# Kernel tuning notes

Measured on AMD Instinct MI355X. Metric: run time of the kernel, lower is better.

## Reference

```python
import jax, jax.numpy as jnp
import numpy as np
import math

B, S, D = 2, 1024, 1024
H, KVH = 16, 4
HD = D // H            # 64
WIN = 256              # sliding window size
E, TOPK = 8, 2
DFF = 4096
T = B * S
CAP = max(1, int(1.0 * T / E))   # capacity_factor=1.0 -> 256
EPS = 1e-6
NEG_INF = float('-inf')


def setup_inputs() -> dict:
    key = jax.random.key(0)
    ks = jax.random.split(key, 10)
    x = jax.random.normal(ks[0], (B, S, D), dtype=jnp.float32)
    # causal additive mask (B,1,S,S)
    i = jnp.arange(S)[:, None]
    j = jnp.arange(S)[None, :]
    causal = jnp.where(j <= i, 0.0, NEG_INF).astype(jnp.float32)
    mask = jnp.broadcast_to(causal[None, None], (B, 1, S, S))
    global_token_mask = jax.random.uniform(ks[1], (B, S)) < 0.05
    sd = 1.0 / math.sqrt(D)
    Wq = jax.random.normal(ks[2], (D, D), jnp.float32) * sd
    Wk = jax.random.normal(ks[3], (D, D), jnp.float32) * sd
    Wv = jax.random.normal(ks[4], (D, D), jnp.float32) * sd
    Wo = jax.random.normal(ks[5], (D, D), jnp.float32) * sd
    g1 = jnp.ones((D,), jnp.float32)
    g2 = jnp.ones((D,), jnp.float32)
    Wgate = jax.random.normal(ks[6], (D, E), jnp.float32) * 0.02
    W1 = jax.random.normal(ks[7], (E, D, 2 * DFF), jnp.float32) * sd
    W2 = jax.random.normal(ks[8], (E, DFF, D), jnp.float32) * (1.0 / math.sqrt(DFF))
    return {"x": x, "mask": mask, "global_token_mask": global_token_mask,
            "Wq": Wq, "Wk": Wk, "Wv": Wv, "Wo": Wo,
            "g1": g1, "g2": g2, "Wgate": Wgate, "W1": W1, "W2": W2}


def _rope_tables():
    inv_freq = 1.0 / (10000.0 ** (jnp.arange(0, HD, 2, dtype=jnp.float32) / HD))
    t = jnp.arange(S, dtype=jnp.float32)
    freqs = t[:, None] * inv_freq[None, :]          # (S, HD/2)
    emb = jnp.concatenate([freqs, freqs], axis=-1)  # (S, HD)
    return emb[None, None].astype(jnp.float32), None  # placeholder


def _rotate_half(x):
    x1, x2 = jnp.split(x, 2, axis=-1)
    return jnp.concatenate([-x2, x1], axis=-1)


def _rmsnorm(x, g):
    return g * x * jax.lax.rsqrt(jnp.mean(x * x, axis=-1, keepdims=True) + EPS)


def _attention(x, mask, gtm, Wq, Wk, Wv, Wo):
    # The torch GQA view/permute chain reduces exactly to a plain head split.
    q = (x @ Wq).reshape(B, S, H, HD).transpose(0, 2, 1, 3)  # (B,H,S,HD)
    k = (x @ Wk).reshape(B, S, H, HD).transpose(0, 2, 1, 3)
    v = (x @ Wv).reshape(B, S, H, HD).transpose(0, 2, 1, 3)
    # inline RoPE
    inv_freq = 1.0 / (10000.0 ** (jnp.arange(0, HD, 2, dtype=jnp.float32) / HD))
    t = jnp.arange(S, dtype=jnp.float32)
    freqs = t[:, None] * inv_freq[None, :]
    emb = jnp.concatenate([freqs, freqs], axis=-1)  # (S,HD)
    cos = jnp.cos(emb)[None, None]
    sin = jnp.sin(emb)[None, None]
    q = q * cos + _rotate_half(q) * sin
    k = k * cos + _rotate_half(k) * sin
    scores = jnp.einsum('bhqd,bhkd->bhqk', q, k) / math.sqrt(HD)
    # sliding-window mask
    i = jnp.arange(S)[:, None]
    j = jnp.arange(S)[None, :]
    diff = i - j
    swa = jnp.where((diff < 0) | (diff >= WIN), NEG_INF, 0.0).astype(scores.dtype)
    combined = mask + swa[None, None]               # (B,1,S,S)
    gt = gtm[:, None, :, None]                      # query is global
    gs = gtm[:, None, None, :]                      # key is global
    combined = jnp.where(gt | gs, 0.0, combined)
    attn = jax.nn.softmax(scores + combined, axis=-1)
    out = jnp.einsum('bhqk,bhkd->bhqd', attn, v)
    out = out.transpose(0, 2, 1, 3).reshape(B, S, D)
    return out @ Wo


def _moe(x, Wgate, W1, W2):
    flat_x = x.reshape(T, D)
    gate_scores = jax.nn.softmax(flat_x @ Wgate, axis=-1)          # (T,E)
    topk_vals, topk_idx = jax.lax.top_k(gate_scores, TOPK)          # (T,k)
    phi_mean = jnp.mean(gate_scores, axis=0)
    aux_loss = E * jnp.sum(phi_mean * phi_mean)
    # per-token weight for each expert (0 if not routed)
    w = jnp.zeros((T, E), flat_x.dtype).at[jnp.arange(T)[:, None], topk_idx].add(topk_vals)
    # capacity: pick top-CAP tokens by weight per expert. Unrouted tokens have
    # weight 0 so any that slip in contribute exactly 0 (matches torch semantics).
    sel_w, sel_idx = jax.lax.top_k(w.T, CAP)                        # (E,CAP)
    tok = flat_x[sel_idx]                                           # (E,CAP,D)
    h = jnp.einsum('ecd,edf->ecf', tok, W1)                         # (E,CAP,2*DFF)
    h1, h2 = jnp.split(h, 2, axis=-1)
    act = h1 * jax.nn.silu(h2)                                      # SwiGLU
    out_e = jnp.einsum('ecf,efd->ecd', act, W2) * sel_w[..., None]
    combined = jnp.zeros((T, D), flat_x.dtype).at[sel_idx.reshape(-1)].add(out_e.reshape(-1, D))
    return combined.reshape(B, S, D), aux_loss


def reference(x, mask, global_token_mask, Wq, Wk, Wv, Wo, g1, g2, Wgate, W1, W2):
    # pre-norm residual block (SublayerConnection with RMSNorm, dropout=identity in eval)
    h = x + _attention(_rmsnorm(x, g1), mask, global_token_mask, Wq, Wk, Wv, Wo)
    moe_out, aux_loss = _moe(_rmsnorm(h, g2), Wgate, W1, W2)
    out = h + moe_out
    return out, aux_loss
```

## Files before the change

### kernel.cpp

```cpp
#include <hip/hip_runtime.h>
#include <hip/hip_bf16.h>
#include <math.h>

#define T_TOK 2048
#define DMODEL 1024
#define NH 16
#define HD 64
#define S_LEN 1024
#define NE 8
#define CAP 256
#define DFF 4096

typedef __attribute__((ext_vector_type(8))) short bf16x8;
typedef __attribute__((ext_vector_type(4))) float f32x4;

__device__ inline unsigned short f2bf(float f) {
    union { float f; unsigned int u; } x; x.f = f;
    unsigned int u = x.u;
    unsigned int r = (u + 0x7FFFu + ((u >> 16) & 1u)) >> 16;
    return (unsigned short)r;
}

__device__ inline float bf2f(unsigned short h) {
    union { unsigned int u; float f; } x; x.u = (unsigned int)h << 16; return x.f;
}

__device__ inline unsigned int pkbf(float lo, float hi) {
    __hip_bfloat162 h2 = __float22bfloat162_rn(make_float2(lo, hi));
    unsigned int r;
    __builtin_memcpy(&r, &h2, 4);
    return r;
}

__device__ inline void gload16(const void* g, void* l) {
    __builtin_amdgcn_global_load_lds(
        (const __attribute__((address_space(1))) unsigned int*)g,
        (__attribute__((address_space(3))) unsigned int*)l, 16, 0, 0);
}

__global__ void rope_table_kernel(float* __restrict__ rc, float* __restrict__ rs,
                                  float* __restrict__ gsum) {
    int s = blockIdx.x;
    int i = threadIdx.x;
    float invf = powf(10000.0f, -(float)(2 * i) / 64.0f);
    float ang = (float)s * invf;
    rc[s * 32 + i] = cosf(ang);
    rs[s * 32 + i] = sinf(ang);
    if (blockIdx.x == 0 && threadIdx.x < 8) gsum[threadIdx.x] = 0.f;
}

template <int OUTBF>
__global__ __launch_bounds__(256) void rmsnorm_kernel(const float* __restrict__ x,
                                                      const float* __restrict__ g,
                                                      void* __restrict__ yv) {
    __shared__ float red[256];
    int t = blockIdx.x;
    int tid = threadIdx.x;
    const float* xr = x + (size_t)t * DMODEL;
    float ss = 0.f;
    for (int d = tid; d < DMODEL; d += 256) { float v = xr[d]; ss += v * v; }
    red[tid] = ss; __syncthreads();
    for (int o = 128; o > 0; o >>= 1) { if (tid < o) red[tid] += red[tid + o]; __syncthreads(); }
    float scale = 1.0f / sqrtf(red[0] / (float)DMODEL + 1e-6f);
    if (OUTBF) {
        unsigned short* yr = (unsigned short*)yv + (size_t)t * DMODEL;
        for (int d = tid; d < DMODEL; d += 256) yr[d] = f2bf(g[d] * xr[d] * scale);
    } else {
        float* yr = (float*)yv + (size_t)t * DMODEL;
        for (int d = tid; d < DMODEL; d += 256) yr[d] = g[d] * xr[d] * scale;
    }
}

__global__ __launch_bounds__(256) void gemm_qkv_rope(const unsigned short* __restrict__ xn,
                                                     const float* __restrict__ Wq,
                                                     const float* __restrict__ Wk,
                                                     const float* __restrict__ Wv,
                                                     const float* __restrict__ rc,
                                                     const float* __restrict__ rs,
                                                     unsigned short* __restrict__ Qh,
                                                     unsigned short* __restrict__ Ql,
                                                     unsigned short* __restrict__ Kh,
                                                     unsigned short* __restrict__ Kl,
                                                     unsigned short* __restrict__ Vtb) {
    __shared__ unsigned short As[128 * 64];
    __shared__ unsigned int Bp[64 * 32];
    const int mat = blockIdx.x >> 4;
    const int h = blockIdx.x & 15;
    const float* B = ((mat == 0) ? Wq : (mat == 1) ? Wk : Wv) + h * 64;
    const int by = blockIdx.y * 128;
    const int tid = threadIdx.x, l = tid & 63, wid = tid >> 6;
    const int g = l >> 4;
    const int kp = tid >> 3;
    const int nc = tid & 7;
    const int chunk = kp >> 2, within = kp & 3;

    f32x4 acc[2][4] = {};

    const float* Brow = B + (size_t)(2 * kp) * 1024 + nc * 8;
    float4 a0 = *(const float4*)(Brow);
    float4 a1 = *(const float4*)(Brow + 4);
    float4 b0 = *(const float4*)(Brow + 1024);
    float4 b1 = *(const float4*)(Brow + 1028);

    for (int k0 = 0; k0 < 1024; k0 += 64) {
        #pragma unroll
        for (int i = 0; i < 4; i++) {
            int c = i * 256 + tid;
            int row = c >> 3, sl = c & 7, gs = sl ^ (row & 7);
            gload16(xn + (size_t)(by + row) * 1024 + k0 + gs * 8, &As[c * 8]);
        }
        unsigned int p[8];
        p[0] = pkbf(a0.x, b0.x); p[1] = pkbf(a0.y, b0.y);
        p[2] = pkbf(a0.z, b0.z); p[3] = pkbf(a0.w, b0.w);
        p[4] = pkbf(a1.x, b1.x); p[5] = pkbf(a1.y, b1.y);
        p[6] = pkbf(a1.z, b1.z); p[7] = pkbf(a1.w, b1.w);
        #pragma unroll
        for (int i = 0; i < 8; i++) {
            int n_loc = nc * 8 + i;
            int idx = n_loc * 32 + ((chunk ^ (n_loc & 7)) << 2) + within;
            Bp[idx] = p[i];
        }
        __syncthreads();
        if (k0 + 64 < 1024) {
            const float* Bn = B + (size_t)(k0 + 64 + 2 * kp) * 1024 + nc * 8;
            a0 = *(const float4*)(Bn);
            a1 = *(const float4*)(Bn + 4);
            b0 = *(const float4*)(Bn + 1024);
            b1 = *(const float4*)(Bn + 1028);
        }
        #pragma unroll
        for (int ks = 0; ks < 2; ks++) {
            bf16x8 af[2];
            #pragma unroll
            for (int m = 0; m < 2; m++) {
                int row = wid * 32 + m * 16 + (l & 15);
                int sl = (ks * 4 + g) ^ (row & 7);
                af[m] = *(const bf16x8*)&As[row * 64 + sl * 8];
            }
            #pragma unroll
            for (int nf = 0; nf < 4; nf++) {
                int n_loc = nf * 16 + (l & 15);
                int base = n_loc * 32 + (((ks * 4 + g) ^ (n_loc & 7)) << 2);
                bf16x8 bfr = *(const bf16x8*)&Bp[base];
                #pragma unroll
                for (int m = 0; m < 2; m++)
                    acc[m][nf] = __builtin_amdgcn_mfma_f32_16x16x32_bf16(af[m], bfr, acc[m][nf], 0, 0, 0);
            }
        }
        __syncthreads();
    }

    if (mat < 2) {
        unsigned short* Dh = (mat == 0) ? Qh : Kh;
        unsigned short* Dl = (mat == 0) ? Ql : Kl;
        float scale = (mat == 0) ? 0.125f : 1.0f;
        #pragma unroll
        for (int m = 0; m < 2; m++)
            #pragma unroll
            for (int r = 0; r < 4; r++) {
                int t = by + wid * 32 + m * 16 + g * 4 + r;
                int b = t >> 10, s = t & 1023;
                size_t ob = ((size_t)(b * 16 + h) * 1024 + s) * 64;
                #pragma unroll
                for (int pr = 0; pr < 2; pr++) {
                    int i = pr * 16 + (l & 15);
                    float c = rc[s * 32 + i], sn = rs[s * 32 + i];
                    float a = acc[m][pr][r], bb = acc[m][pr + 2][r];
                    float v0 = (a * c - bb * sn) * scale;
                    float v1 = (bb * c + a * sn) * scale;
                    unsigned short h0 = f2bf(v0), h1 = f2bf(v1);
                    Dh[ob + i] = h0;      Dl[ob + i] = f2bf(v0 - bf2f(h0));
                    Dh[ob + i + 32] = h1; Dl[ob + i + 32] = f2bf(v1 - bf2f(h1));
                }
            }
    } else {
        #pragma unroll
        for (int m = 0; m < 2; m++) {
            int t0 = by + wid * 32 + m * 16 + g * 4;
            int b = t0 >> 10, s0 = t0 & 1023;
            #pragma unroll
            for (int nf = 0; nf < 4; nf++) {
                int d = nf * 16 + (l & 15);
                unsigned short tmp[4];
                #pragma unroll
                for (int r = 0; r < 4; r++) tmp[r] = f2bf(acc[m][nf][r]);
                *(uint2*)&Vtb[((size_t)(b * 16 + h) * 64 + d) * 1024 + s0] = *(uint2*)tmp;
            }
        }
    }
}

template <int RES>
__global__ __launch_bounds__(256) void gemm_bf32(const unsigned short* __restrict__ A,
                                                 const float* __restrict__ B,
                                                 const float* __restrict__ Rr,
                                                 float* __restrict__ C,
                                                 int K, int lda,
                                                 long long sA, long long sB, long long sC) {
    __shared__ unsigned short As[128 * 64];
    __shared__ unsigned int Bp[32 * 32];
    A += (long long)blockIdx.z * sA + (long long)blockIdx.y * 128 * lda;
    B += (long long)blockIdx.z * sB;
    C += (long long)blockIdx.z * sC + (long long)blockIdx.y * 128 * 1024;
    const float* Rp = RES ? (Rr + (long long)blockIdx.y * 128 * 1024) : nullptr;
    const int bx = blockIdx.x * 32;
    const int tid = threadIdx.x, l = tid & 63, wid = tid >> 6;
    const int g = l >> 4;
    const int kp = tid >> 3;
    const int nc = tid & 7;
    const int chunk = kp >> 2, within = kp & 3;

    f32x4 acc[2][2] = {};

    const float* Brow = B + (size_t)(2 * kp) * 1024 + bx + nc * 4;
    float4 a0 = *(const float4*)(Brow);
    float4 a1 = *(const float4*)(Brow + 1024);

    for (int k0 = 0; k0 < K; k0 += 64) {
        #pragma unroll
        for (int i = 0; i < 4; i++) {
            int c = i * 256 + tid;
            int row = c >> 3, sl = c & 7, gs = sl ^ (row & 7);
            gload16(A + (size_t)row * lda + k0 + gs * 8, &As[c * 8]);
        }
        unsigned int p1[4];
        p1[0] = pkbf(a0.x, a1.x); p1[1] = pkbf(a0.y, a1.y);
        p1[2] = pkbf(a0.z, a1.z); p1[3] = pkbf(a0.w, a1.w);
        #pragma unroll
        for (int i = 0; i < 4; i++) {
            int n_loc = nc * 4 + i;
            int idx = n_loc * 32 + ((chunk ^ (n_loc & 7)) << 2) + within;
            Bp[idx] = p1[i];
        }
        __syncthreads();
        if (k0 + 64 < K) {
            const float* Bn = B + (size_t)(k0 + 64 + 2 * kp) * 1024 + bx + nc * 4;
            a0 = *(const float4*)(Bn);
            a1 = *(const float4*)(Bn + 1024);
        }
        #pragma unroll
        for (int ks = 0; ks < 2; ks++) {
            bf16x8 af[2];
            #pragma unroll
            for (int m = 0; m < 2; m++) {
                int row = wid * 32 + m * 16 + (l & 15);
                int sl = (ks * 4 + g) ^ (row & 7);
                af[m] = *(const bf16x8*)&As[row * 64 + sl * 8];
            }
            #pragma unroll
            for (int nf = 0; nf < 2; nf++) {
                int n_loc = nf * 16 + (l & 15);
                int base = n_loc * 32 + (((ks * 4 + g) ^ (n_loc & 7)) << 2);
                bf16x8 bfr = *(const bf16x8*)&Bp[base];
                #pragma unroll
                for (int m = 0; m < 2; m++)
                    acc[m][nf] = __builtin_amdgcn_mfma_f32_16x16x32_bf16(af[m], bfr, acc[m][nf], 0, 0, 0);
            }
        }
        __syncthreads();
    }
    #pragma unroll
    for (int m = 0; m < 2; m++) {
        int row0 = wid * 32 + m * 16 + g * 4;
        #pragma unroll
        for (int nf = 0; nf < 2; nf++) {
            int col = bx + nf * 16 + (l & 15);
            #pragma unroll
            for (int r = 0; r < 4; r++) {
                size_t idx = (size_t)(row0 + r) * 1024 + col;
                float v = acc[m][nf][r];
                if (RES) v += Rp[idx];
                C[idx] = v;
            }
        }
    }
}

__global__ __launch_bounds__(256) void gemm_w1_fused(const unsigned short* __restrict__ tok,
                                                     const float* __restrict__ W1,
                                                     unsigned short* __restrict__ act) {
    __shared__ unsigned short As[256 * 64];
    __shared__ unsigned int B1p[32 * 32];
    __shared__ unsigned int B2p[32 * 32];
    const int e = blockIdx.y;
    const int bx = blockIdx.x * 32;
    const unsigned short* A = tok + (size_t)e * CAP * DMODEL;
    const float* B = W1 + (size_t)e * DMODEL * (2 * DFF);
    unsigned short* C = act + (size_t)e * CAP * DFF;
    const int tid = threadIdx.x, l = tid & 63, wid = tid >> 6;
    const int g = l >> 4;
    const int kp = tid >> 3;
    const int nc = tid & 7;
    const int chunk = kp >> 2, within = kp & 3;

    f32x4 acc1[4][2] = {};
    f32x4 acc2[4][2] = {};

    const float* Brow = B + (size_t)(2 * kp) * 8192 + bx + nc * 4;
    float4 a0 = *(const float4*)(Brow);
    float4 a1 = *(const float4*)(Brow + 8192);
    float4 c0 = *(const float4*)(Brow + 4096);
    float4 c1 = *(const float4*)(Brow + 4096 + 8192);

    for (int k0 = 0; k0 < DMODEL; k0 += 64) {
        #pragma unroll
        for (int i = 0; i < 8; i++) {
            int c = i * 256 + tid;
            int row = c >> 3, sl = c & 7, gs = sl ^ (row & 7);
            gload16(A + (size_t)row * DMODEL + k0 + gs * 8, &As[c * 8]);
        }
        unsigned int p1[4], p2[4];
        p1[0] = pkbf(a0.x, a1.x); p1[1] = pkbf(a0.y, a1.y);
        p1[2] = pkbf(a0.z, a1.z); p1[3] = pkbf(a0.w, a1.w);
        p2[0] = pkbf(c0.x, c1.x); p2[1] = pkbf(c0.y, c1.y);
        p2[2] = pkbf(c0.z, c1.z); p2[3] = pkbf(c0.w, c1.w);
        #pragma unroll
        for (int i = 0; i < 4; i++) {
            int n_loc = nc * 4 + i;
            int idx = n_loc * 32 + ((chunk ^ (n_loc & 7)) << 2) + within;
            B1p[idx] = p1[i];
            B2p[idx] = p2[i];
        }
        __syncthreads();
        if (k0 + 64 < DMODEL) {
            const float* Bn = B + (size_t)(k0 + 64 + 2 * kp) * 8192 + bx + nc * 4;
            a0 = *(const float4*)(Bn);
            a1 = *(const float4*)(Bn + 8192);
            c0 = *(const float4*)(Bn + 4096);
            c1 = *(const float4*)(Bn + 4096 + 8192);
        }
        #pragma unroll
        for (int ks = 0; ks < 2; ks++) {
            bf16x8 af[4];
            #pragma unroll
            for (int m = 0; m < 4; m++) {
                int row = wid * 64 + m * 16 + (l & 15);
                int sl = (ks * 4 + g) ^ (row & 7);
                af[m] = *(const bf16x8*)&As[row * 64 + sl * 8];
            }
            #pragma unroll
            for (int nf = 0; nf < 2; nf++) {
                int n_loc = nf * 16 + (l & 15);
                int base = n_loc * 32 + (((ks * 4 + g) ^ (n_loc & 7)) << 2);
                bf16x8 b1 = *(const bf16x8*)&B1p[base];
                bf16x8 b2 = *(const bf16x8*)&B2p[base];
                #pragma unroll
                for (int m = 0; m < 4; m++) {
                    acc1[m][nf] = __builtin_amdgcn_mfma_f32_16x16x32_bf16(af[m], b1, acc1[m][nf], 0, 0, 0);
                    acc2[m][nf] = __builtin_amdgcn_mfma_f32_16x16x32_bf16(af[m], b2, acc2[m][nf], 0, 0, 0);
                }
            }
        }
        __syncthreads();
    }
    #pragma unroll
    for (int m = 0; m < 4; m++) {
        int row0 = wid * 64 + m * 16 + g * 4;
        #pragma unroll
        for (int nf = 0; nf < 2; nf++) {
            int col = bx + nf * 16 + (l & 15);
            #pragma unroll
            for (int r = 0; r < 4; r++) {
                float h1 = acc1[m][nf][r], h2 = acc2[m][nf][r];
                float sil = h2 / (1.0f + __expf(-h2));
                C[(size_t)(row0 + r) * DFF + col] = f2bf(h1 * sil);
            }
        }
    }
}

__global__ __launch_bounds__(256) void attn_mfma_kernel(const unsigned short* __restrict__ Qh,
                                                        const unsigned short* __restrict__ Ql,
                                                        const unsigned short* __restrict__ Kh,
                                                        const unsigned short* __restrict__ Kl,
                                                        const unsigned short* __restrict__ Vtb,
                                                        const int* __restrict__ gtm,
                                                        unsigned short* __restrict__ o) {
    __shared__ unsigned short Ksh[2][64 * 64];
    __shared__ unsigned short Ksl[2][64 * 64];
    __shared__ unsigned short Vs[2][64 * 64];
    __shared__ unsigned short Pl[4][16 * 64];
    const int qt = blockIdx.x, h = blockIdx.y, b = blockIdx.z;
    const int bh = b * 16 + h;
    const int tid = threadIdx.x, l = tid & 63, w = tid >> 6;
    const int q0 = qt * 64 + w * 16;
    const unsigned short* Qhb = Qh + (size_t)bh * 1024 * 64;
    const unsigned short* Qlb = Ql + (size_t)bh * 1024 * 64;
    const unsigned short* Khb = Kh + (size_t)bh * 1024 * 64;
    const unsigned short* Klb = Kl + (size_t)bh * 1024 * 64;
    const unsigned short* Vbh = Vtb + (size_t)bh * 64 * 1024;
    const int* gb = gtm + b * 1024;

    bf16x8 afh[2], afl[2];
    #pragma unroll
    for (int ks = 0; ks < 2; ks++) {
        size_t off = (size_t)(q0 + (l & 15)) * 64 + ks * 32 + (l >> 4) * 8;
        afh[ks] = *(const bf16x8*)(Qhb + off);
        afl[ks] = *(const bf16x8*)(Qlb + off);
    }

    int gqm = 0;
    #pragma unroll
    for (int r = 0; r < 4; r++)
        gqm |= (gb[q0 + (l >> 4) * 4 + r] ? 1 : 0) << r;

    f32x4 acc_o[4] = {};
    float m_run[4], l_run[4];
    #pragma unroll
    for (int r = 0; r < 4; r++) { m_run[r] = -1e30f; l_run[r] = 0.f; }

    {
        #pragma unroll
        for (int i = 0; i < 2; i++) {
            int c = i * 256 + tid, row = c >> 3, sl = c & 7, gs = sl ^ (row & 7);
            gload16(Khb + (size_t)row * 64 + gs * 8, &Ksh[0][c * 8]);
            gload16(Klb + (size_t)row * 64 + gs * 8, &Ksl[0][c * 8]);
            gload16(Vbh + (size_t)row * 1024 + gs * 8, &Vs[0][c * 8]);
        }
    }
    int cur = 0;

    for (int jt = 0; jt < 16; jt++) {
        const int j0 = jt * 64;
        __syncthreads();

        if (jt < 15) {
            const int jn = j0 + 64;
            int nb = cur ^ 1;
            #pragma unroll
            for (int i = 0; i < 2; i++) {
                int c = i * 256 + tid, row = c >> 3, sl = c & 7, gs = sl ^ (row & 7);
                gload16(Khb + (size_t)(jn + row) * 64 + gs * 8, &Ksh[nb][c * 8]);
                gload16(Klb + (size_t)(jn + row) * 64 + gs * 8, &Ksl[nb][c * 8]);
                gload16(Vbh + (size_t)row * 1024 + jn + gs * 8, &Vs[nb][c * 8]);
            }
        }

        f32x4 sv[4] = {};
        __builtin_amdgcn_s_setprio(1);
        #pragma unroll
        for (int n = 0; n < 4; n++) {
            #pragma unroll
            for (int ks = 0; ks < 2; ks++) {
                int row = n * 16 + (l & 15);
                int sl = (ks * 4 + (l >> 4)) ^ (row & 7);
                bf16x8 khf = *(const bf16x8*)&Ksh[cur][row * 64 + sl * 8];
                bf16x8 klf = *(const bf16x8*)&Ksl[cur][row * 64 + sl * 8];
                sv[n] = __builtin_amdgcn_mfma_f32_16x16x32_bf16(afl[ks], khf, sv[n], 0, 0, 0);
                sv[n] = __builtin_amdgcn_mfma_f32_16x16x32_bf16(afh[ks], klf, sv[n], 0, 0, 0);
                sv[n] = __builtin_amdgcn_mfma_f32_16x16x32_bf16(afh[ks], khf, sv[n], 0, 0, 0);
            }
        }
        __builtin_amdgcn_s_setprio(0);

        int gk[4];
        #pragma unroll
        for (int n = 0; n < 4; n++) gk[n] = gb[j0 + n * 16 + (l & 15)];

        #pragma unroll
        for (int n = 0; n < 4; n++)
            #pragma unroll
            for (int r = 0; r < 4; r++) {
                int q = q0 + (l >> 4) * 4 + r;
                int k = j0 + n * 16 + (l & 15);
                bool allowed = ((gqm >> r) & 1) || gk[n] || ((k <= q) && (q - k < 256));
                if (!allowed) sv[n][r] = -1e30f;
            }

        {
            float tm[4], corr[4], rsum[4];
            #pragma unroll
            for (int r = 0; r < 4; r++)
                tm[r] = fmaxf(fmaxf(sv[0][r], sv[1][r]), fmaxf(sv[2][r], sv[3][r]));
            #pragma unroll
            for (int wd = 1; wd <= 8; wd <<= 1)
                #pragma unroll
                for (int r = 0; r < 4; r++) tm[r] = fmaxf(tm[r], __shfl_xor(tm[r], wd, 64));
            #pragma unroll
            for (int r = 0; r < 4; r++) {
                float mn = fmaxf(m_run[r], tm[r]);
                corr[r] = __expf(m_run[r] - mn);
                m_run[r] = mn;
                rsum[r] = 0.f;
            }
            #pragma unroll
            for (int n = 0; n < 4; n++)
                #pragma unroll
                for (int r = 0; r < 4; r++) {
                    float p = __expf(sv[n][r] - m_run[r]);
                    sv[n][r] = p;
                    rsum[r] += p;
                }
            #pragma unroll
            for (int wd = 1; wd <= 8; wd <<= 1)
                #pragma unroll
                for (int r = 0; r < 4; r++) rsum[r] += __shfl_xor(rsum[r], wd, 64);
            #pragma unroll
            for (int r = 0; r < 4; r++) l_run[r] = l_run[r] * corr[r] + rsum[r];
            #pragma unroll
            for (int nd = 0; nd < 4; nd++)
                #pragma unroll
                for (int r = 0; r < 4; r++) acc_o[nd][r] *= corr[r];
            #pragma unroll
            for (int n = 0; n < 4; n++)
                #pragma unroll
                for (int r = 0; r < 4; r++) {
                    int qr = (l >> 4) * 4 + r;
                    int kc = n * 16 + (l & 15);
                    int byte = (qr * 128 + kc * 2) ^ ((qr & 7) << 4);
                    Pl[w][byte >> 1] = f2bf(sv[n][r]);
                }
        }

        asm volatile("s_waitcnt lgkmcnt(0)" ::: "memory");
        __builtin_amdgcn_sched_barrier(0);

        __builtin_amdgcn_s_setprio(1);
        #pragma unroll
        for (int ks = 0; ks < 2; ks++) {
            int prow = l & 15;
            int psl = (ks * 4 + (l >> 4)) ^ (prow & 7);
            bf16x8 pa = *(const bf16x8*)&Pl[w][prow * 64 + psl * 8];
            #pragma unroll
            for (int nd = 0; nd < 4; nd++) {
                int row = nd * 16 + (l & 15);
                int sl = (ks * 4 + (l >> 4)) ^ (row & 7);
                bf16x8 vf = *(const bf16x8*)&Vs[cur][row * 64 + sl * 8];
                acc_o[nd] = __builtin_amdgcn_mfma_f32_16x16x32_bf16(pa, vf, acc_o[nd], 0, 0, 0);
            }
        }
        __builtin_amdgcn_s_setprio(0);
        cur ^= 1;
    }

    #pragma unroll
    for (int r = 0; r < 4; r++) {
        float inv = 1.0f / l_run[r];
        int t_ = b * 1024 + q0 + (l >> 4) * 4 + r;
        #pragma unroll
        for (int nd = 0; nd < 4; nd++) {
            int col = h * 64 + nd * 16 + (l & 15);
            o[(size_t)t_ * 1024 + col] = f2bf(acc_o[nd][r] * inv);
        }
    }
}

__global__ __launch_bounds__(256) void gate_kernel(const float* __restrict__ hn,
                                                   const float* __restrict__ Wgate,
                                                   float* __restrict__ wfull,
                                                   int* __restrict__ slot,
                                                   float* __restrict__ gate_sum) {
    int tid = threadIdx.x;
    int w = tid >> 6, l = tid & 63;
    int t = blockIdx.x * 4 + w;
    int e = l & 7, g = l >> 3;
    const float* xr = hn + (size_t)t * DMODEL;
    const float* wp = Wgate + l;
    float acc = 0.f;
    #pragma unroll 8
    for (int kk = 0; kk < 128; kk++)
        acc += xr[g + 8 * kk] * wp[64 * kk];
    #pragma unroll
    for (int o = 8; o < 64; o <<= 1) acc += __shfl_xor(acc, o, 64);
    float m = acc;
    #pragma unroll
    for (int o = 1; o < 8; o <<= 1) m = fmaxf(m, __shfl_xor(m, o, 64));
    float p = __expf(acc - m);
    float s = p;
    #pragma unroll
    for (int o = 1; o < 8; o <<= 1) s += __shfl_xor(s, o, 64);
    float pr = p / s;
    unsigned long long key = ((unsigned long long)__float_as_uint(pr) << 32) | (unsigned)(7 - e);
    unsigned long long k1 = key;
    #pragma unroll
    for (int o = 1; o < 8; o <<= 1) { unsigned long long t2 = __shfl_xor(k1, o, 64); if (t2 > k1) k1 = t2; }
    int e1 = 7 - (int)(k1 & 7);
    unsigned long long key2 = (e == e1) ? 0ull : key;
    unsigned long long k2 = key2;
    #pragma unroll
    for (int o = 1; o < 8; o <<= 1) { unsigned long long t2 = __shfl_xor(k2, o, 64); if (t2 > k2) k2 = t2; }
    int e2 = 7 - (int)(k2 & 7);
    if (l < 8) {
        wfull[t * 8 + e] = (e == e1 || e == e2) ? pr : 0.f;
        slot[t * 8 + e] = -1;
        atomicAdd(&gate_sum[e], pr);
    }
}

__global__ __launch_bounds__(1024) void expert_select_kernel(const float* __restrict__ wfull,
                                                             float* __restrict__ sw,
                                                             int* __restrict__ sidx,
                                                             int* __restrict__ slot) {
    __shared__ unsigned long long keys[2048];
    int e = blockIdx.x;
    int t = threadIdx.x;
    for (int i = t; i < 2048; i += 1024) {
        float w = wfull[i * 8 + e];
        unsigned int wb = __float_as_uint(w);
        keys[i] = ((unsigned long long)wb << 32) | (unsigned long long)(0xFFFFFFFFu - (unsigned int)i);
    }
    __syncthreads();
    for (int k = 2; k <= 2048; k <<= 1) {
        for (int j = k >> 1; j > 0; j >>= 1) {
            for (int i = t; i < 2048; i += 1024) {
                int ixj = i ^ j;
                if (ixj > i) {
                    bool desc = ((i & k) == 0);
                    unsigned long long a = keys[i], b = keys[ixj];
                    if ((a < b) == desc) { keys[i] = b; keys[ixj] = a; }
                }
            }
            __syncthreads();
        }
    }
    if (t < CAP) {
        unsigned long long kk = keys[t];
        float w = __uint_as_float((unsigned int)(kk >> 32));
        int idx = (int)(0xFFFFFFFFu - (unsigned int)(kk & 0xFFFFFFFFu));
        sw[e * CAP + t] = w;
        sidx[e * CAP + t] = idx;
        if (w > 0.f) slot[idx * 8 + e] = t;
    }
}

__global__ __launch_bounds__(256) void gather_tok_kernel(const float* __restrict__ hn,
                                                         const int* __restrict__ sidx,
                                                         const float* __restrict__ sw,
                                                         unsigned short* __restrict__ tok) {
    int ec = blockIdx.x;
    int tid = threadIdx.x;
    float w = sw[ec];
    int src = sidx[ec];
    const float* s = hn + (size_t)src * DMODEL;
    unsigned short* d = tok + (size_t)ec * DMODEL;
    for (int i = tid; i < DMODEL; i += 256) d[i] = (w > 0.f) ? f2bf(s[i]) : 0;
}

__global__ __launch_bounds__(256) void combine_kernel(const float* __restrict__ h,
                                                      const float* __restrict__ out_e,
                                                      const int* __restrict__ slot,
                                                      const float* __restrict__ wfull,
                                                      const float* __restrict__ gate_sum,
                                                      float* __restrict__ out) {
    int t = blockIdx.x;
    int tid = threadIdx.x;
    for (int d = tid; d < DMODEL; d += 256) {
        float acc = h[(size_t)t * DMODEL + d];
        #pragma unroll
        for (int e = 0; e < 8; e++) {
            int c = slot[t * 8 + e];
            if (c >= 0) acc += wfull[t * 8 + e] * out_e[((size_t)(e * CAP + c)) * DMODEL + d];
        }
        out[(size_t)t * DMODEL + d] = acc;
    }
    if (t == 0 && tid == 0) {
        float a = 0.f;
        #pragma unroll
        for (int e = 0; e < 8; e++) { float m = gate_sum[e] / (float)T_TOK; a += m * m; }
        out[(size_t)T_TOK * DMODEL] = 8.0f * a;
    }
}

extern "C" void kernel_launch(void* const* d_in, const int* in_sizes, int n_in,
                              void* d_out, int out_size, void* d_ws, size_t ws_size,
                              hipStream_t stream) {
    const float* x     = (const float*)d_in[0];
    const int*   gtm   = (const int*)d_in[2];
    const float* Wq    = (const float*)d_in[3];
    const float* Wk    = (const float*)d_in[4];
    const float* Wv    = (const float*)d_in[5];
    const float* Wo    = (const float*)d_in[6];
    const float* g1    = (const float*)d_in[7];
    const float* g2    = (const float*)d_in[8];
    const float* Wgate = (const float*)d_in[9];
    const float* W1    = (const float*)d_in[10];
    const float* W2    = (const float*)d_in[11];
    float* out = (float*)d_out;

    char* ws = (char*)d_ws;
    unsigned short* Qh   = (unsigned short*)(ws + 0);
    unsigned short* Ql   = (unsigned short*)(ws + 4194304);
    unsigned short* Kh   = (unsigned short*)(ws + 8388608);
    unsigned short* Kl   = (unsigned short*)(ws + 12582912);
    unsigned short* Vtb  = (unsigned short*)(ws + 16777216);
    unsigned short* act  = (unsigned short*)(ws + 0);
    unsigned short* xn   = (unsigned short*)(ws + 20971520);
    unsigned short* attno= (unsigned short*)(ws + 25165824);
    float* hb    = (float*)(ws + 29360128);
    float* hnb   = (float*)(ws + 37748736);
    float* oute  = (float*)(ws + 46137344);
    unsigned short* tok = (unsigned short*)(ws + 54525952);
    float* ropec = (float*)(ws + 58720256);
    float* ropes = (float*)(ws + 58851328);
    float* wfull = (float*)(ws + 58982400);
    int*   slot  = (int*)(ws + 59047936);
    float* sw    = (float*)(ws + 59113472);
    int*   sidx  = (int*)(ws + 59121664);
    float* gsum  = (float*)(ws + 59129856);

    rope_table_kernel<<<S_LEN, 32, 0, stream>>>(ropec, ropes, gsum);
    rmsnorm_kernel<1><<<T_TOK, 256, 0, stream>>>(x, g1, xn);

    gemm_qkv_rope<<<dim3(48, 16, 1), 256, 0, stream>>>(
        xn, Wq, Wk, Wv, ropec, ropes, Qh, Ql, Kh, Kl, Vtb);

    attn_mfma_kernel<<<dim3(16, 16, 2), 256, 0, stream>>>(Qh, Ql, Kh, Kl, Vtb, gtm, attno);

    gemm_bf32<1><<<dim3(32, 16, 1), 256, 0, stream>>>(
        attno, Wo, x, hb, 1024, 1024, 0, 0, 0);
    rmsnorm_kernel<0><<<T_TOK, 256, 0, stream>>>(hb, g2, hnb);

    gate_kernel<<<T_TOK / 4, 256, 0, stream>>>(hnb, Wgate, wfull, slot, gsum);
    expert_select_kernel<<<NE, 1024, 0, stream>>>(wfull, sw, sidx, slot);
    gather_tok_kernel<<<NE * CAP, 256, 0, stream>>>(hnb, sidx, sw, tok);

    gemm_w1_fused<<<dim3(128, 8, 1), 256, 0, stream>>>(tok, W1, act);
    gemm_bf32<0><<<dim3(32, 2, 8), 256, 0, stream>>>(
        act, W2, nullptr, oute, 4096, 4096,
        (long long)CAP * DFF, (long long)DFF * 1024, (long long)CAP * 1024);

    combine_kernel<<<T_TOK, 256, 0, stream>>>(hb, oute, slot, wfull, gsum, out);
}
```

Baseline: 353.5 us.

## Restrict attention to sliding window plus gathered global keys, add fixup pass

Attention now visits only the key tiles inside the 256-token causal window plus up to two tiles of compacted global-token keys, instead of all 16 key tiles for every query block. A scan kernel compacts global token indices, and a gather kernel copies their K/V into a dense buffer. A separate fixup kernel recomputes full attention rows for global query tokens. The second RMSNorm is also fused with the gating softmax and top-2. This adds small kernels and caps global tokens at 128 per batch, which could be wrong if more exist.

```diff
diff --git a/kernel.cpp b/kernel.cpp
--- a/kernel.cpp
+++ b/kernel.cpp
@@ -49,10 +49,30 @@
     if (blockIdx.x == 0 && threadIdx.x < 8) gsum[threadIdx.x] = 0.f;
 }
 
-template <int OUTBF>
+__global__ __launch_bounds__(1024) void gscan_kernel(const int* __restrict__ gtm,
+                                                     int* __restrict__ gidx,
+                                                     int* __restrict__ gcnt) {
+    __shared__ int ps[1024];
+    int b = blockIdx.x, t = threadIdx.x;
+    int f = gtm[b * 1024 + t] ? 1 : 0;
+    ps[t] = f;
+    __syncthreads();
+    for (int off = 1; off < 1024; off <<= 1) {
+        int v = (t >= off) ? ps[t - off] : 0;
+        __syncthreads();
+        ps[t] += v;
+        __syncthreads();
+    }
+    if (f) {
+        int pos = ps[t] - 1;
+        if (pos < 128) gidx[b * 128 + pos] = t;
+    }
+    if (t == 1023) gcnt[b] = ps[1023] > 128 ? 128 : ps[1023];
+}
+
 __global__ __launch_bounds__(256) void rmsnorm_kernel(const float* __restrict__ x,
                                                       const float* __restrict__ g,
-                                                      void* __restrict__ yv) {
+                                                      unsigned short* __restrict__ y) {
     __shared__ float red[256];
     int t = blockIdx.x;
     int tid = threadIdx.x;
@@ -62,12 +82,71 @@
     red[tid] = ss; __syncthreads();
     for (int o = 128; o > 0; o >>= 1) { if (tid < o) red[tid] += red[tid + o]; __syncthreads(); }
     float scale = 1.0f / sqrtf(red[0] / (float)DMODEL + 1e-6f);
-    if (OUTBF) {
-        unsigned short* yr = (unsigned short*)yv + (size_t)t * DMODEL;
-        for (int d = tid; d < DMODEL; d += 256) yr[d] = f2bf(g[d] * xr[d] * scale);
-    } else {
-        float* yr = (float*)yv + (size_t)t * DMODEL;
-        for (int d = tid; d < DMODEL; d += 256) yr[d] = g[d] * xr[d] * scale;
+    unsigned short* yr = y + (size_t)t * DMODEL;
+    for (int d = tid; d < DMODEL; d += 256) yr[d] = f2bf(g[d] * xr[d] * scale);
+}
+
+__global__ __launch_bounds__(256) void rmsnorm_gate_kernel(const float* __restrict__ x,
+                                                           const float* __restrict__ g,
+                                                           const float* __restrict__ Wgate,
+                                                           float* __restrict__ y,
+                                                           float* __restrict__ wfull,
+                                                           int* __restrict__ slot,
+                                                           float* __restrict__ gate_sum) {
+    __shared__ float red[256];
+    __shared__ float lg[8];
+    int t = blockIdx.x, tid = threadIdx.x;
+    const float* xr = x + (size_t)t * DMODEL;
+    float xv[4]; float ss = 0.f;
+    #pragma unroll
+    for (int i = 0; i < 4; i++) { xv[i] = xr[tid + i * 256]; ss += xv[i] * xv[i]; }
+    red[tid] = ss; __syncthreads();
+    for (int o = 128; o > 0; o >>= 1) { if (tid < o) red[tid] += red[tid + o]; __syncthreads(); }
+    float scale = 1.0f / sqrtf(red[0] / (float)DMODEL + 1e-6f);
+    float part[8] = {};
+    float* yr = y + (size_t)t * DMODEL;
+    #pragma unroll
+    for (int i = 0; i < 4; i++) {
+        int d = tid + i * 256;
+        float yv = g[d] * xv[i] * scale;
+        yr[d] = yv;
+        const float* wg = Wgate + d * 8;
+        #pragma unroll
+        for (int e = 0; e < 8; e++) part[e] += yv * wg[e];
+    }
+    __syncthreads();
+    for (int e = 0; e < 8; e++) {
+        red[tid] = part[e]; __syncthreads();
+        for (int o = 128; o > 0; o >>= 1) { if (tid < o) red[tid] += red[tid + o]; __syncthreads(); }
+        if (tid == 0) lg[e] = red[0];
+        __syncthreads();
+    }
+    if (tid == 0) {
+        float mx = lg[0];
+        #pragma unroll
+        for (int e = 1; e < 8; e++) mx = fmaxf(mx, lg[e]);
+        float pr[8]; float s = 0.f;
+        #pragma unroll
+        for (int e = 0; e < 8; e++) { pr[e] = __expf(lg[e] - mx); s += pr[e]; }
+        float inv = 1.0f / s;
+        int e1 = 0; float v1 = -1.f;
+        #pragma unroll
+        for (int e = 0; e < 8; e++) {
+            pr[e] *= inv;
+            atomicAdd(&gate_sum[e], pr[e]);
+            if (pr[e] > v1) { v1 = pr[e]; e1 = e; }
+        }
+        int e2 = -1; float v2 = -1.f;
+        #pragma unroll
+        for (int e = 0; e < 8; e++) {
+            if (e == e1) continue;
+            if (pr[e] > v2) { v2 = pr[e]; e2 = e; }
+        }
+        #pragma unroll
+        for (int e = 0; e < 8; e++) {
+            wfull[t * 8 + e] = (e == e1) ? v1 : (e == e2) ? v2 : 0.f;
+            slot[t * 8 + e] = -1;
+        }
     }
 }
 
@@ -190,6 +269,309 @@
     }
 }
 
+__global__ __launch_bounds__(256) void gather_gkv_kernel(const unsigned short* __restrict__ Kh,
+                                                         const unsigned short* __restrict__ Kl,
+                                                         const unsigned short* __restrict__ Vtb,
+                                                         const int* __restrict__ gidx,
+                                                         const int* __restrict__ gcnt,
+                                                         unsigned short* __restrict__ Kgh,
+                                                         unsigned short* __restrict__ Kgl,
+                                                         unsigned short* __restrict__ Vgt) {
+    int bh = blockIdx.x;
+    int b = bh >> 4;
+    int cnt = gcnt[b];
+    int tid = threadIdx.x;
+    for (int i = tid; i < 128 * 8; i += 256) {
+        int slot = i >> 3, c8 = (i & 7) * 8;
+        size_t dst = ((size_t)bh * 128 + slot) * 64 + c8;
+        if (slot < cnt) {
+            int idx = gidx[b * 128 + slot];
+            size_t src = ((size_t)bh * 1024 + idx) * 64 + c8;
+            *(uint4*)(Kgh + dst) = *(const uint4*)(Kh + src);
+            *(uint4*)(Kgl + dst) = *(const uint4*)(Kl + src);
+        } else {
+            uint4 z = {0, 0, 0, 0};
+            *(uint4*)(Kgh + dst) = z;
+            *(uint4*)(Kgl + dst) = z;
+        }
+    }
+    for (int i = tid; i < 64 * 16; i += 256) {
+        int d = i >> 4, s8 = (i & 15) * 8;
+        unsigned short tmp[8];
+        #pragma unroll
+        for (int u = 0; u < 8; u++) {
+            int slot = s8 + u;
+            tmp[u] = (slot < cnt) ? Vtb[((size_t)bh * 64 + d) * 1024 + gidx[b * 128 + slot]]
+                                  : (unsigned short)0;
+        }
+        *(uint4*)(Vgt + ((size_t)bh * 64 + d) * 128 + s8) = *(uint4*)tmp;
+    }
+}
+
+__global__ __launch_bounds__(256) void attn_mfma_kernel(const unsigned short* __restrict__ Qh,
+                                                        const unsigned short* __restrict__ Ql,
+                                                        const unsigned short* __restrict__ Kh,
+                                                        const unsigned short* __restrict__ Kl,
+                                                        const unsigned short* __restrict__ Vtb,
+                                                        const unsigned short* __restrict__ Kgh,
+                                                        const unsigned short* __restrict__ Kgl,
+                                                        const unsigned short* __restrict__ Vgt,
+                                                        const int* __restrict__ gtm,
+                                                        const int* __restrict__ gcnt,
+                                                        unsigned short* __restrict__ o) {
+    __shared__ unsigned short Ksh[2][64 * 64];
+    __shared__ unsigned short Ksl[2][64 * 64];
+    __shared__ unsigned short Vs[2][64 * 64];
+    __shared__ unsigned short Pl[4][16 * 64];
+    const int qt = blockIdx.x, h = blockIdx.y, b = blockIdx.z;
+    const int bh = b * 16 + h;
+    const int tid = threadIdx.x, l = tid & 63, w = tid >> 6;
+    const int q0 = qt * 64 + w * 16;
+    const int jt_lo = (qt >= 4) ? (qt - 4) : 0;
+    const int nwin = qt - jt_lo + 1;
+    const int ntiles = nwin + 2;
+    const int cnt = gcnt[b];
+    const unsigned short* Qhb = Qh + (size_t)bh * 1024 * 64;
+    const unsigned short* Qlb = Ql + (size_t)bh * 1024 * 64;
+    const unsigned short* Khb = Kh + (size_t)bh * 1024 * 64;
+    const unsigned short* Klb = Kl + (size_t)bh * 1024 * 64;
+    const unsigned short* Vbh = Vtb + (size_t)bh * 64 * 1024;
+    const unsigned short* Kghb = Kgh + (size_t)bh * 128 * 64;
+    const unsigned short* Kglb = Kgl + (size_t)bh * 128 * 64;
+    const unsigned short* Vgtb = Vgt + (size_t)bh * 64 * 128;
+    const int* gb = gtm + b * 1024;
+
+    bf16x8 afh[2], afl[2];
+    #pragma unroll
+    for (int ks = 0; ks < 2; ks++) {
+        size_t off = (size_t)(q0 + (l & 15)) * 64 + ks * 32 + (l >> 4) * 8;
+        afh[ks] = *(const bf16x8*)(Qhb + off);
+        afl[ks] = *(const bf16x8*)(Qlb + off);
+    }
+
+    f32x4 acc_o[4] = {};
+    float m_run[4], l_run[4];
+    #pragma unroll
+    for (int r = 0; r < 4; r++) { m_run[r] = -1e30f; l_run[r] = 0.f; }
+
+    auto STAGE = [&](int ti, int buf) {
+        if (ti < nwin) {
+            int j0s = (jt_lo + ti) * 64;
+            #pragma unroll
+            for (int i = 0; i < 2; i++) {
+                int c = i * 256 + tid, row = c >> 3, sl = c & 7, gs = sl ^ (row & 7);
+                gload16(Khb + (size_t)(j0s + row) * 64 + gs * 8, &Ksh[buf][c * 8]);
+                gload16(Klb + (size_t)(j0s + row) * 64 + gs * 8, &Ksl[buf][c * 8]);
+                gload16(Vbh + (size_t)row * 1024 + j0s + gs * 8, &Vs[buf][c * 8]);
+            }
+        } else {
+            int g0 = (ti - nwin) * 64;
+            #pragma unroll
+            for (int i = 0; i < 2; i++) {
+                int c = i * 256 + tid, row = c >> 3, sl = c & 7, gs = sl ^ (row & 7);
+                gload16(Kghb + (size_t)(g0 + row) * 64 + gs * 8, &Ksh[buf][c * 8]);
+                gload16(Kglb + (size_t)(g0 + row) * 64 + gs * 8, &Ksl[buf][c * 8]);
+                gload16(Vgtb + (size_t)row * 128 + g0 + gs * 8, &Vs[buf][c * 8]);
+            }
+        }
+    };
+
+    STAGE(0, 0);
+    int cur = 0;
+
+    for (int ti = 0; ti < ntiles; ti++) {
+        __syncthreads();
+        if (ti + 1 < ntiles) STAGE(ti + 1, cur ^ 1);
+
+        f32x4 sv[4] = {};
+        __builtin_amdgcn_s_setprio(1);
+        #pragma unroll
+        for (int n = 0; n < 4; n++) {
+            #pragma unroll
+            for (int ks = 0; ks < 2; ks++) {
+                int row = n * 16 + (l & 15);
+                int sl = (ks * 4 + (l >> 4)) ^ (row & 7);
+                bf16x8 khf = *(const bf16x8*)&Ksh[cur][row * 64 + sl * 8];
+                bf16x8 klf = *(const bf16x8*)&Ksl[cur][row * 64 + sl * 8];
+                sv[n] = __builtin_amdgcn_mfma_f32_16x16x32_bf16(afl[ks], khf, sv[n], 0, 0, 0);
+                sv[n] = __builtin_amdgcn_mfma_f32_16x16x32_bf16(afh[ks], klf, sv[n], 0, 0, 0);
+                sv[n] = __builtin_amdgcn_mfma_f32_16x16x32_bf16(afh[ks], khf, sv[n], 0, 0, 0);
+            }
+        }
+        __builtin_amdgcn_s_setprio(0);
+
+        if (ti < nwin) {
+            int j0 = (jt_lo + ti) * 64;
+            int gk[4];
+            #pragma unroll
+            for (int n = 0; n < 4; n++) gk[n] = gb[j0 + n * 16 + (l & 15)];
+            #pragma unroll
+            for (int n = 0; n < 4; n++)
+                #pragma unroll
+                for (int r = 0; r < 4; r++) {
+                    int q = q0 + (l >> 4) * 4 + r;
+                    int k = j0 + n * 16 + (l & 15);
+                    bool allowed = (k <= q) && (q - k < 256) && !gk[n];
+                    if (!allowed) sv[n][r] = -1e30f;
+                }
+        } else {
+            int s0 = (ti - nwin) * 64;
+            #pragma unroll
+            for (int n = 0; n < 4; n++) {
+                int slot = s0 + n * 16 + (l & 15);
+                bool allowed = slot < cnt;
+                #pragma unroll
+                for (int r = 0; r < 4; r++)
+                    if (!allowed) sv[n][r] = -1e30f;
+            }
+        }
+
+        {
+            float tm[4], corr[4], rsum[4];
+            #pragma unroll
+            for (int r = 0; r < 4; r++)
+                tm[r] = fmaxf(fmaxf(sv[0][r], sv[1][r]), fmaxf(sv[2][r], sv[3][r]));
+            #pragma unroll
+            for (int wd = 1; wd <= 8; wd <<= 1)
+                #pragma unroll
+                for (int r = 0; r < 4; r++) tm[r] = fmaxf(tm[r], __shfl_xor(tm[r], wd, 64));
+            #pragma unroll
+            for (int r = 0; r < 4; r++) {
+                float mn = fmaxf(m_run[r], tm[r]);
+                corr[r] = __expf(m_run[r] - mn);
+                m_run[r] = mn;
+                rsum[r] = 0.f;
+            }
+            #pragma unroll
+            for (int n = 0; n < 4; n++)
+                #pragma unroll
+                for (int r = 0; r < 4; r++) {
+                    float p = __expf(sv[n][r] - m_run[r]);
+                    sv[n][r] = p;
+                    rsum[r] += p;
+                }
+            #pragma unroll
+            for (int wd = 1; wd <= 8; wd <<= 1)
+                #pragma unroll
+                for (int r = 0; r < 4; r++) rsum[r] += __shfl_xor(rsum[r], wd, 64);
+            #pragma unroll
+            for (int r = 0; r < 4; r++) l_run[r] = l_run[r] * corr[r] + rsum[r];
+            #pragma unroll
+            for (int nd = 0; nd < 4; nd++)
+                #pragma unroll
+                for (int r = 0; r < 4; r++) acc_o[nd][r] *= corr[r];
+            #pragma unroll
+            for (int n = 0; n < 4; n++)
+                #pragma unroll
+                for (int r = 0; r < 4; r++) {
+                    int qr = (l >> 4) * 4 + r;
+                    int kc = n * 16 + (l & 15);
+                    int byte = (qr * 128 + kc * 2) ^ ((qr & 7) << 4);
+                    Pl[w][byte >> 1] = f2bf(sv[n][r]);
+                }
+        }
+
+        asm volatile("s_waitcnt lgkmcnt(0)" ::: "memory");
+        __builtin_amdgcn_sched_barrier(0);
+
+        __builtin_amdgcn_s_setprio(1);
+        #pragma unroll
+        for (int ks = 0; ks < 2; ks++) {
+            int prow = l & 15;
+            int psl = (ks * 4 + (l >> 4)) ^ (prow & 7);
+            bf16x8 pa = *(const bf16x8*)&Pl[w][prow * 64 + psl * 8];
+            #pragma unroll
+            for (int nd = 0; nd < 4; nd++) {
+                int row = nd * 16 + (l & 15);
+                int sl = (ks * 4 + (l >> 4)) ^ (row & 7);
+                bf16x8 vf = *(const bf16x8*)&Vs[cur][row * 64 + sl * 8];
+                acc_o[nd] = __builtin_amdgcn_mfma_f32_16x16x32_bf16(pa, vf, acc_o[nd], 0, 0, 0);
+            }
+        }
+        __builtin_amdgcn_s_setprio(0);
+        cur ^= 1;
+    }
+
+    #pragma unroll
+    for (int r = 0; r < 4; r++) {
+        float inv = 1.0f / l_run[r];
+        int t_ = b * 1024 + q0 + (l >> 4) * 4 + r;
+        #pragma unroll
+        for (int nd = 0; nd < 4; nd++) {
+            int col = h * 64 + nd * 16 + (l & 15);
+            o[(size_t)t_ * 1024 + col] = f2bf(acc_o[nd][r] * inv);
+        }
+    }
+}
+
+__global__ __launch_bounds__(256) void attn_fixup_kernel(const unsigned short* __restrict__ Qh,
+                                                         const unsigned short* __restrict__ Ql,
+                                                         const unsigned short* __restrict__ Kh,
+                                                         const unsigned short* __restrict__ Kl,
+                                                         const unsigned short* __restrict__ Vtb,
+                                                         const int* __restrict__ gidx,
+                                                         const int* __restrict__ gcnt,
+                                                         unsigned short* __restrict__ o) {
+    int slot = blockIdx.x, h = blockIdx.y, b = blockIdx.z;
+    if (slot >= gcnt[b]) return;
+    int t = gidx[b * 128 + slot];
+    int bh = b * 16 + h;
+    __shared__ float qf[64];
+    __shared__ float sc[1024];
+    __shared__ float red[256];
+    __shared__ float pacc[4][64];
+    int tid = threadIdx.x;
+    if (tid < 64) {
+        size_t qo = ((size_t)bh * 1024 + t) * 64 + tid;
+        qf[tid] = bf2f(Qh[qo]) + bf2f(Ql[qo]);
+    }
+    __syncthreads();
+    float myS[4];
+    #pragma unroll
+    for (int jj = 0; jj < 4; jj++) {
+        int k = jj * 256 + tid;
+        const uint4* kh4 = (const uint4*)(Kh + ((size_t)bh * 1024 + k) * 64);
+        const uint4* kl4 = (const uint4*)(Kl + ((size_t)bh * 1024 + k) * 64);
+        float acc = 0.f;
+        #pragma unroll
+        for (int c = 0; c < 8; c++) {
+            union { uint4 v; unsigned short s[8]; } uh, ul;
+            uh.v = kh4[c]; ul.v = kl4[c];
+            #pragma unroll
+            for (int u = 0; u < 8; u++)
+                acc += qf[c * 8 + u] * (bf2f(uh.s[u]) + bf2f(ul.s[u]));
+        }
+        myS[jj] = acc;
+    }
+    float m = fmaxf(fmaxf(myS[0], myS[1]), fmaxf(myS[2], myS[3]));
+    red[tid] = m; __syncthreads();
+    for (int off = 128; off > 0; off >>= 1) { if (tid < off) red[tid] = fmaxf(red[tid], red[tid + off]); __syncthreads(); }
+    m = red[0]; __syncthreads();
+    float s = 0.f;
+    #pragma unroll
+    for (int jj = 0; jj < 4; jj++) {
+        float p = __expf(myS[jj] - m);
+        sc[jj * 256 + tid] = p;
+        s += p;
+    }
+    red[tid] = s; __syncthreads();
+    for (int off = 128; off > 0; off >>= 1) { if (tid < off) red[tid] += red[tid + off]; __syncthreads(); }
+    float inv = 1.0f / red[0];
+    __syncthreads();
+    int dd = tid & 63, jg = tid >> 6;
+    const unsigned short* vrow = Vtb + ((size_t)bh * 64 + dd) * 1024;
+    float acc = 0.f;
+    for (int i = 0; i < 256; i++) {
+        int j = jg * 256 + i;
+        acc += sc[j] * bf2f(vrow[j]);
+    }
+    pacc[jg][dd] = acc; __syncthreads();
+    if (tid < 64) {
+        float sum = pacc[0][tid] + pacc[1][tid] + pacc[2][tid] + pacc[3][tid];
+        o[((size_t)(b * 1024 + t)) * 1024 + h * 64 + tid] = f2bf(sum * inv);
+    }
+}
+
 template <int RES>
 __global__ __launch_bounds__(256) void gemm_bf32(const unsigned short* __restrict__ A,
                                                  const float* __restrict__ B,
@@ -366,224 +748,6 @@
                 C[(size_t)(row0 + r) * DFF + col] = f2bf(h1 * sil);
             }
         }
-    }
-}
-
-__global__ __launch_bounds__(256) void attn_mfma_kernel(const unsigned short* __restrict__ Qh,
-                                                        const unsigned short* __restrict__ Ql,
-                                                        const unsigned short* __restrict__ Kh,
-                                                        const unsigned short* __restrict__ Kl,
-                                                        const unsigned short* __restrict__ Vtb,
-                                                        const int* __restrict__ gtm,
-                                                        unsigned short* __restrict__ o) {
-    __shared__ unsigned short Ksh[2][64 * 64];
-    __shared__ unsigned short Ksl[2][64 * 64];
-    __shared__ unsigned short Vs[2][64 * 64];
-    __shared__ unsigned short Pl[4][16 * 64];
-    const int qt = blockIdx.x, h = blockIdx.y, b = blockIdx.z;
-    const int bh = b * 16 + h;
-    const int tid = threadIdx.x, l = tid & 63, w = tid >> 6;
-    const int q0 = qt * 64 + w * 16;
-    const unsigned short* Qhb = Qh + (size_t)bh * 1024 * 64;
-    const unsigned short* Qlb = Ql + (size_t)bh * 1024 * 64;
-    const unsigned short* Khb = Kh + (size_t)bh * 1024 * 64;
-    const unsigned short* Klb = Kl + (size_t)bh * 1024 * 64;
-    const unsigned short* Vbh = Vtb + (size_t)bh * 64 * 1024;
-    const int* gb = gtm + b * 1024;
-
-    bf16x8 afh[2], afl[2];
-    #pragma unroll
-    for (int ks = 0; ks < 2; ks++) {
-        size_t off = (size_t)(q0 + (l & 15)) * 64 + ks * 32 + (l >> 4) * 8;
-        afh[ks] = *(const bf16x8*)(Qhb + off);
-        afl[ks] = *(const bf16x8*)(Qlb + off);
-    }
-
-    int gqm = 0;
-    #pragma unroll
-    for (int r = 0; r < 4; r++)
-        gqm |= (gb[q0 + (l >> 4) * 4 + r] ? 1 : 0) << r;
-
-    f32x4 acc_o[4] = {};
-    float m_run[4], l_run[4];
-    #pragma unroll
-    for (int r = 0; r < 4; r++) { m_run[r] = -1e30f; l_run[r] = 0.f; }
-
-    {
-        #pragma unroll
-        for (int i = 0; i < 2; i++) {
-            int c = i * 256 + tid, row = c >> 3, sl = c & 7, gs = sl ^ (row & 7);
-            gload16(Khb + (size_t)row * 64 + gs * 8, &Ksh[0][c * 8]);
-            gload16(Klb + (size_t)row * 64 + gs * 8, &Ksl[0][c * 8]);
-            gload16(Vbh + (size_t)row * 1024 + gs * 8, &Vs[0][c * 8]);
-        }
-    }
-    int cur = 0;
-
-    for (int jt = 0; jt < 16; jt++) {
-        const int j0 = jt * 64;
-        __syncthreads();
-
-        if (jt < 15) {
-            const int jn = j0 + 64;
-            int nb = cur ^ 1;
-            #pragma unroll
-            for (int i = 0; i < 2; i++) {
-                int c = i * 256 + tid, row = c >> 3, sl = c & 7, gs = sl ^ (row & 7);
-                gload16(Khb + (size_t)(jn + row) * 64 + gs * 8, &Ksh[nb][c * 8]);
-                gload16(Klb + (size_t)(jn + row) * 64 + gs * 8, &Ksl[nb][c * 8]);
-                gload16(Vbh + (size_t)row * 1024 + jn + gs * 8, &Vs[nb][c * 8]);
-            }
-        }
-
-        f32x4 sv[4] = {};
-        __builtin_amdgcn_s_setprio(1);
-        #pragma unroll
-        for (int n = 0; n < 4; n++) {
-            #pragma unroll
-            for (int ks = 0; ks < 2; ks++) {
-                int row = n * 16 + (l & 15);
-                int sl = (ks * 4 + (l >> 4)) ^ (row & 7);
-                bf16x8 khf = *(const bf16x8*)&Ksh[cur][row * 64 + sl * 8];
-                bf16x8 klf = *(const bf16x8*)&Ksl[cur][row * 64 + sl * 8];
-                sv[n] = __builtin_amdgcn_mfma_f32_16x16x32_bf16(afl[ks], khf, sv[n], 0, 0, 0);
-                sv[n] = __builtin_amdgcn_mfma_f32_16x16x32_bf16(afh[ks], klf, sv[n], 0, 0, 0);
-                sv[n] = __builtin_amdgcn_mfma_f32_16x16x32_bf16(afh[ks], khf, sv[n], 0, 0, 0);
-            }
-        }
-        __builtin_amdgcn_s_setprio(0);
-
-        int gk[4];
-        #pragma unroll
-        for (int n = 0; n < 4; n++) gk[n] = gb[j0 + n * 16 + (l & 15)];
-
-        #pragma unroll
-        for (int n = 0; n < 4; n++)
-            #pragma unroll
-            for (int r = 0; r < 4; r++) {
-                int q = q0 + (l >> 4) * 4 + r;
-                int k = j0 + n * 16 + (l & 15);
-                bool allowed = ((gqm >> r) & 1) || gk[n] || ((k <= q) && (q - k < 256));
-                if (!allowed) sv[n][r] = -1e30f;
-            }
-
-        {
-            float tm[4], corr[4], rsum[4];
-            #pragma unroll
-            for (int r = 0; r < 4; r++)
-                tm[r] = fmaxf(fmaxf(sv[0][r], sv[1][r]), fmaxf(sv[2][r], sv[3][r]));
-            #pragma unroll
-            for (int wd = 1; wd <= 8; wd <<= 1)
-                #pragma unroll
-                for (int r = 0; r < 4; r++) tm[r] = fmaxf(tm[r], __shfl_xor(tm[r], wd, 64));
-            #pragma unroll
-            for (int r = 0; r < 4; r++) {
-                float mn = fmaxf(m_run[r], tm[r]);
-                corr[r] = __expf(m_run[r] - mn);
-                m_run[r] = mn;
-                rsum[r] = 0.f;
-            }
-            #pragma unroll
-            for (int n = 0; n < 4; n++)
-                #pragma unroll
-                for (int r = 0; r < 4; r++) {
-                    float p = __expf(sv[n][r] - m_run[r]);
-                    sv[n][r] = p;
-                    rsum[r] += p;
-                }
-            #pragma unroll
-            for (int wd = 1; wd <= 8; wd <<= 1)
-                #pragma unroll
-                for (int r = 0; r < 4; r++) rsum[r] += __shfl_xor(rsum[r], wd, 64);
-            #pragma unroll
-            for (int r = 0; r < 4; r++) l_run[r] = l_run[r] * corr[r] + rsum[r];
-            #pragma unroll
-            for (int nd = 0; nd < 4; nd++)
-                #pragma unroll
-                for (int r = 0; r < 4; r++) acc_o[nd][r] *= corr[r];
-            #pragma unroll
-            for (int n = 0; n < 4; n++)
-                #pragma unroll
-                for (int r = 0; r < 4; r++) {
-                    int qr = (l >> 4) * 4 + r;
-                    int kc = n * 16 + (l & 15);
-                    int byte = (qr * 128 + kc * 2) ^ ((qr & 7) << 4);
-                    Pl[w][byte >> 1] = f2bf(sv[n][r]);
-                }
-        }
-
-        asm volatile("s_waitcnt lgkmcnt(0)" ::: "memory");
-        __builtin_amdgcn_sched_barrier(0);
-
-        __builtin_amdgcn_s_setprio(1);
-        #pragma unroll
-        for (int ks = 0; ks < 2; ks++) {
-            int prow = l & 15;
-            int psl = (ks * 4 + (l >> 4)) ^ (prow & 7);
-            bf16x8 pa = *(const bf16x8*)&Pl[w][prow * 64 + psl * 8];
-            #pragma unroll
-            for (int nd = 0; nd < 4; nd++) {
-                int row = nd * 16 + (l & 15);
-                int sl = (ks * 4 + (l >> 4)) ^ (row & 7);
-                bf16x8 vf = *(const bf16x8*)&Vs[cur][row * 64 + sl * 8];
-                acc_o[nd] = __builtin_amdgcn_mfma_f32_16x16x32_bf16(pa, vf, acc_o[nd], 0, 0, 0);
-            }
-        }
-        __builtin_amdgcn_s_setprio(0);
-        cur ^= 1;
-    }
-
-    #pragma unroll
-    for (int r = 0; r < 4; r++) {
-        float inv = 1.0f / l_run[r];
-        int t_ = b * 1024 + q0 + (l >> 4) * 4 + r;
-        #pragma unroll
-        for (int nd = 0; nd < 4; nd++) {
-            int col = h * 64 + nd * 16 + (l & 15);
-            o[(size_t)t_ * 1024 + col] = f2bf(acc_o[nd][r] * inv);
-        }
-    }
-}
-
-__global__ __launch_bounds__(256) void gate_kernel(const float* __restrict__ hn,
-                                                   const float* __restrict__ Wgate,
-                                                   float* __restrict__ wfull,
-                                                   int* __restrict__ slot,
-                                                   float* __restrict__ gate_sum) {
-    int tid = threadIdx.x;
-    int w = tid >> 6, l = tid & 63;
-    int t = blockIdx.x * 4 + w;
-    int e = l & 7, g = l >> 3;
-    const float* xr = hn + (size_t)t * DMODEL;
-    const float* wp = Wgate + l;
-    float acc = 0.f;
-    #pragma unroll 8
-    for (int kk = 0; kk < 128; kk++)
-        acc += xr[g + 8 * kk] * wp[64 * kk];
-    #pragma unroll
-    for (int o = 8; o < 64; o <<= 1) acc += __shfl_xor(acc, o, 64);
-    float m = acc;
-    #pragma unroll
-    for (int o = 1; o < 8; o <<= 1) m = fmaxf(m, __shfl_xor(m, o, 64));
-    float p = __expf(acc - m);
-    float s = p;
-    #pragma unroll
-    for (int o = 1; o < 8; o <<= 1) s += __shfl_xor(s, o, 64);
-    float pr = p / s;
-    unsigned long long key = ((unsigned long long)__float_as_uint(pr) << 32) | (unsigned)(7 - e);
-    unsigned long long k1 = key;
-    #pragma unroll
-    for (int o = 1; o < 8; o <<= 1) { unsigned long long t2 = __shfl_xor(k1, o, 64); if (t2 > k1) k1 = t2; }
-    int e1 = 7 - (int)(k1 & 7);
-    unsigned long long key2 = (e == e1) ? 0ull : key;
-    unsigned long long k2 = key2;
-    #pragma unroll
-    for (int o = 1; o < 8; o <<= 1) { unsigned long long t2 = __shfl_xor(k2, o, 64); if (t2 > k2) k2 = t2; }
-    int e2 = 7 - (int)(k2 & 7);
-    if (l < 8) {
-        wfull[t * 8 + e] = (e == e1 || e == e2) ? pr : 0.f;
-        slot[t * 8 + e] = -1;
-        atomicAdd(&gate_sum[e], pr);
     }
 }
 
@@ -697,20 +861,31 @@
     float* sw    = (float*)(ws + 59113472);
     int*   sidx  = (int*)(ws + 59121664);
     float* gsum  = (float*)(ws + 59129856);
+    int*   gidx  = (int*)(ws + 59131904);
+    int*   gcnt  = (int*)(ws + 59133952);
+    unsigned short* Kgh = (unsigned short*)(ws + 59140096);
+    unsigned short* Kgl = (unsigned short*)(ws + 59664384);
+    unsigned short* Vgt = (unsigned short*)(ws + 60188672);
 
     rope_table_kernel<<<S_LEN, 32, 0, stream>>>(ropec, ropes, gsum);
-    rmsnorm_kernel<1><<<T_TOK, 256, 0, stream>>>(x, g1, xn);
+    gscan_kernel<<<2, 1024, 0, stream>>>(gtm, gidx, gcnt);
+    rmsnorm_kernel<<<T_TOK, 256, 0, stream>>>(x, g1, xn);
 
     gemm_qkv_rope<<<dim3(48, 16, 1), 256, 0, stream>>>(
         xn, Wq, Wk, Wv, ropec, ropes, Qh, Ql, Kh, Kl, Vtb);
 
-    attn_mfma_kernel<<<dim3(16, 16, 2), 256, 0, stream>>>(Qh, Ql, Kh, Kl, Vtb, gtm, attno);
+    gather_gkv_kernel<<<32, 256, 0, stream>>>(Kh, Kl, Vtb, gidx, gcnt, Kgh, Kgl, Vgt);
+
+    attn_mfma_kernel<<<dim3(16, 16, 2), 256, 0, stream>>>(
+        Qh, Ql, Kh, Kl, Vtb, Kgh, Kgl, Vgt, gtm, gcnt, attno);
+
+    attn_fixup_kernel<<<dim3(128, 16, 2), 256, 0, stream>>>(
+        Qh, Ql, Kh, Kl, Vtb, gidx, gcnt, attno);
 
     gemm_bf32<1><<<dim3(32, 16, 1), 256, 0, stream>>>(
         attno, Wo, x, hb, 1024, 1024, 0, 0, 0);
-    rmsnorm_kernel<0><<<T_TOK, 256, 0, stream>>>(hb, g2, hnb);
-
-    gate_kernel<<<T_TOK / 4, 256, 0, stream>>>(hnb, Wgate, wfull, slot, gsum);
+
+    rmsnorm_gate_kernel<<<T_TOK, 256, 0, stream>>>(hb, g2, Wgate, hnb, wfull, slot, gsum);
     expert_select_kernel<<<NE, 1024, 0, stream>>>(wfull, sw, sidx, slot);
     gather_tok_kernel<<<NE * CAP, 256, 0, stream>>>(hnb, sidx, sw, tok);
 
```

Measured after the change: 734.1 us. +107.6%, slower.
